# Performance work log

Measured on AMD Instinct MI355X. Metric: run time of the kernel, lower is better.

## Reference

```python
import jax, jax.numpy as jnp
import numpy as np

N_ENT = 50000
N_REL = 500
N_EDGE = 640000
D_IN = 128
D_OUT = 128
NEG_SLOPE = 0.01  # torch nn.LeakyReLU default
BN_EPS = 1e-5


def setup_inputs() -> dict:
    key = jax.random.key(0)
    ks = jax.random.split(key, 16)
    edge_index = jax.random.randint(ks[0], (2, N_EDGE), 0, N_ENT)
    edge_type = jax.random.randint(ks[1], (N_EDGE,), 0, N_REL)
    query_type = jax.random.randint(ks[2], (N_EDGE,), 0, N_REL)
    entity_embed = jax.random.normal(ks[3], (N_ENT, D_IN), jnp.float32)
    rel_embed = jax.random.normal(ks[4], (N_REL, D_IN), jnp.float32)
    s = 0.05
    return {
        "edge_index": edge_index,
        "edge_type": edge_type,
        "query_type": query_type,
        "entity_embed": entity_embed,
        "rel_embed": rel_embed,
        "w_loop": jax.random.normal(ks[5], (D_IN, D_OUT), jnp.float32) * s,
        "w_out": jax.random.normal(ks[6], (D_IN, D_OUT), jnp.float32) * s,
        "w_rel": jax.random.normal(ks[7], (D_IN, D_OUT), jnp.float32) * s,
        "loop_rel": jax.random.normal(ks[8], (1, D_IN), jnp.float32) * s,
        "W_w": jax.random.normal(ks[9], (D_IN, D_IN), jnp.float32) * s,   # W.weight^T layout: x @ W_w
        "W_b": jnp.zeros((D_IN,), jnp.float32),
        "a_w": jax.random.normal(ks[10], (2 * D_IN, 1), jnp.float32) * s,
        "a_b": jnp.zeros((1,), jnp.float32),
        "bias": jnp.zeros((D_OUT,), jnp.float32),
        "bn_gamma": jnp.ones((D_OUT,), jnp.float32),
        "bn_beta": jnp.zeros((D_OUT,), jnp.float32),
    }


def _compgcn_fwd(edge_index, edge_type, query_type, entity_embed, rel_embed,
                 w_loop, w_out, w_rel, loop_rel, W_w, W_b, a_w, a_b,
                 bias, bn_gamma, bn_beta):
    N = entity_embed.shape[0]
    rel_all = jnp.concatenate([rel_embed, loop_rel], axis=0)  # (R+1, D)
    row, col = edge_index[0], edge_index[1]  # values already in [0, N)

    # edge norm: 1/out-degree of source node (deg[row] >= 1 for every edge)
    deg = jax.ops.segment_sum(jnp.ones((row.shape[0],), entity_embed.dtype), row, num_segments=N)
    norm = 1.0 / deg[row]  # (E,)

    # self-loop branch (mode='loop'): rel_transform 'mult' with loop relation, no attention
    loop_res = (entity_embed * rel_all[-1]) @ w_loop  # (N, D_out)

    # out branch (mode='out')
    x_j = entity_embed[col]          # (E, D)
    r_e = rel_all[edge_type]         # (E, D)
    q_e = rel_all[query_type]        # (E, D)
    xj_rel = x_j * r_e               # 'mult' composition

    h = jnp.concatenate([r_e @ W_w + W_b, q_e @ W_w + W_b], axis=-1)  # (E, 2D)
    logits = h @ a_w + a_b                                            # (E, 1)
    alpha = jnp.exp(jax.nn.leaky_relu(logits[:, 0], NEG_SLOPE))       # (E,)
    sum_alpha = jax.ops.segment_sum(alpha, row, num_segments=N)       # (N,)
    alpha = alpha / sum_alpha[row]

    msg = (xj_rel @ w_out) * (alpha * norm)[:, None]                  # (E, D_out)
    out_res = jax.ops.segment_sum(msg, row, num_segments=N)           # (N, D_out)

    out = 0.5 * out_res + 0.5 * loop_res + bias  # dropout = identity (eval)
    # BatchNorm1d, training-mode batch statistics (biased var), over node dim
    mean = jnp.mean(out, axis=0)
    var = jnp.mean((out - mean) ** 2, axis=0)
    out = (out - mean) * jax.lax.rsqrt(var + BN_EPS) * bn_gamma + bn_beta

    ent_out = jax.nn.leaky_relu(out, NEG_SLOPE)
    rel_out = (rel_all @ w_rel)[:-1]
    return ent_out, rel_out


def reference(edge_index, edge_type, query_type, entity_embed, rel_embed,
              w_loop, w_out, w_rel, loop_rel, W_w, W_b, a_w, a_b,
              bias, bn_gamma, bn_beta):
    return _compgcn_fwd(edge_index, edge_type, query_type, entity_embed, rel_embed,
                        w_loop, w_out, w_rel, loop_rel, W_w, W_b, a_w, a_b,
                        bias, bn_gamma, bn_beta)
```

## Files before the change

kernel.cpp:

```cpp
#include <hip/hip_runtime.h>
#include <math.h>

#define E_N 640000
#define N_N 50000
#define R_N 500
#define D   128
#define NEG 0.01f
#define BNEPS 1e-5f
#define CAP 48
#define GROUPS 8
#define RPG 6250

typedef __bf16 bf16x8 __attribute__((ext_vector_type(8)));
typedef float f32x4 __attribute__((ext_vector_type(4)));

#define CNT_OFF    0u
#define STAT_OFF   50000u
#define ZERO_FLOATS 50256u
#define BUCKET_OFF 50256u
#define ENTBF_OFF  4850256u
#define RELBF_OFF  8050256u
#define BT_OFF     8082256u
#define S1_OFF     8098640u
#define S2_OFF     8099152u

__device__ __forceinline__ float lrelu(float x) { return x > 0.f ? x : NEG * x; }

__device__ __forceinline__ void st_bf16x4(__bf16* p, float x, float y, float z, float w) {
    union { __bf16 b[4]; uint2 u; } pk;
    pk.b[0] = (__bf16)x; pk.b[1] = (__bf16)y; pk.b[2] = (__bf16)z; pk.b[3] = (__bf16)w;
    *(uint2*)p = pk.u;
}

__device__ __forceinline__ void st_bf16x8(__bf16* p, const float* v) {
    union { __bf16 b[8]; uint4 u; } pk;
#pragma unroll
    for (int j = 0; j < 8; ++j) pk.b[j] = (__bf16)v[j];
    *(uint4*)p = pk.u;
}

__device__ __forceinline__ void fma8(uint4 ue, uint4 ur, float a, float* acc) {
    const unsigned* we = (const unsigned*)&ue;
    const unsigned* wr = (const unsigned*)&ur;
#pragma unroll
    for (int w = 0; w < 4; ++w) {
        float e_lo = __uint_as_float(we[w] << 16);
        float e_hi = __uint_as_float(we[w] & 0xffff0000u);
        float r_lo = __uint_as_float(wr[w] << 16);
        float r_hi = __uint_as_float(wr[w] & 0xffff0000u);
        acc[2 * w]     = fmaf(a * e_lo, r_lo, acc[2 * w]);
        acc[2 * w + 1] = fmaf(a * e_hi, r_hi, acc[2 * w + 1]);
    }
}

#define P1_S   501
#define P1_WB  256
#define P1_REL 500
#define P1_ENT 1563

__global__ __launch_bounds__(128) void k_pre1(const float* __restrict__ Ww,
                                              const float* __restrict__ Wb,
                                              const float* __restrict__ aw,
                                              const float* __restrict__ rel,
                                              const float* __restrict__ looprel,
                                              const float* __restrict__ wout,
                                              const float* __restrict__ wloop,
                                              const float* __restrict__ wrel,
                                              const float* __restrict__ ent,
                                              float* __restrict__ s1,
                                              float* __restrict__ s2,
                                              __bf16* __restrict__ Bt,
                                              float* __restrict__ out_rel,
                                              __bf16* __restrict__ rel_bf,
                                              __bf16* __restrict__ ent_bf) {
    int b = blockIdx.x, t = threadIdx.x;
    if (b < P1_S) {
        __shared__ float rr[D];
        __shared__ float part[4];
        const float* rp = (b < R_N) ? rel + (size_t)b * D : looprel;
        rr[t] = rp[t];
        if (b < R_N) rel_bf[(size_t)b * D + t] = (__bf16)rp[t];
        __syncthreads();
        float v = 0.f;
        for (int i = 0; i < D; ++i) v = fmaf(rr[i], Ww[i * D + t], v);
        float p1 = aw[t] * v + Wb[t] * aw[t];
        float p2 = aw[D + t] * v + Wb[t] * aw[D + t];
        for (int o = 32; o; o >>= 1) {
            p1 += __shfl_down(p1, o);
            p2 += __shfl_down(p2, o);
        }
        if ((t & 63) == 0) {
            part[(t >> 6) * 2] = p1;
            part[(t >> 6) * 2 + 1] = p2;
        }
        __syncthreads();
        if (t == 0) {
            s1[b] = part[0] + part[2];
            s2[b] = part[1] + part[3];
        }
    } else if (b < P1_S + P1_WB) {
        int idx = (b - P1_S) * 128 + t;
        int n = idx & 127, k = idx >> 7;
        float v = (k < D) ? wout[(size_t)k * D + n] : wloop[(size_t)(k - D) * D + n];
        Bt[(size_t)n * 256 + k] = (__bf16)v;
    } else if (b < P1_S + P1_WB + P1_REL) {
        int r = b - (P1_S + P1_WB);
        __shared__ float rr2[D];
        rr2[t] = rel[(size_t)r * D + t];
        __syncthreads();
        float a = 0.f;
        for (int k = 0; k < D; ++k) a = fmaf(rr2[k], wrel[(size_t)k * D + t], a);
        out_rel[(size_t)r * D + t] = a;
    } else {
        int blk = b - (P1_S + P1_WB + P1_REL);
        const float4* e4 = (const float4*)ent;
#pragma unroll
        for (int j = 0; j < 8; ++j) {
            int idx = blk * 1024 + j * 128 + t;
            if (idx < N_N * D / 4) {
                float4 v = e4[idx];
                st_bf16x4(ent_bf + (size_t)idx * 4, v.x, v.y, v.z, v.w);
            }
        }
    }
}

#define BIN_BLOCKS (625 * GROUPS)

__global__ __launch_bounds__(256) void k_bin(const int* __restrict__ row,
                                             const int* __restrict__ col,
                                             const int* __restrict__ et,
                                             const int* __restrict__ qt,
                                             const float* __restrict__ s1,
                                             const float* __restrict__ s2,
                                             const float* __restrict__ ab,
                                             int* __restrict__ cnt,
                                             int2* __restrict__ bucket) {
    int b = blockIdx.x, t = threadIdx.x;
    int g = b & 7;
    int chunk = b >> 3;
    int rlo = g * RPG;
    int e0 = chunk * 1024 + t;
    int r[4];
#pragma unroll
    for (int j = 0; j < 4; ++j) r[j] = row[e0 + j * 256];
#pragma unroll
    for (int j = 0; j < 4; ++j) {
        unsigned rr = (unsigned)(r[j] - rlo);
        if (rr < RPG) {
            int e = e0 + j * 256;
            int c = col[e], te = et[e], q = qt[e];
            float a = __expf(lrelu(s1[te] + s2[q] + ab[0]));
            int pos = atomicAdd(&cnt[r[j]], 1);
            if (pos < CAP) {
                bucket[(size_t)r[j] * CAP + pos] =
                    make_int2(c | (te << 16), __float_as_int(a));
            }
        }
    }
}

__global__ __launch_bounds__(128) void k_gather(const int* __restrict__ cnt,
                                                const int2* __restrict__ bucket,
                                                const __bf16* __restrict__ ent_bf,
                                                const __bf16* __restrict__ rel_bf,
                                                const float* __restrict__ looprel,
                                                __bf16* __restrict__ stage) {
    int n = (blockIdx.x & 7) * RPG + (blockIdx.x >> 3);
    int t = threadIdx.x;
    int deg = cnt[n];
    int m = deg < CAP ? deg : CAP;
    __shared__ int eoff[CAP];
    __shared__ int roff[CAP];
    __shared__ float sa[CAP];
    __shared__ float xred[16][8];
    if (t < CAP) {
        if (t < m) {
            int2 be = bucket[(size_t)n * CAP + t];
            eoff[t] = (be.x & 0xffff) << 8;
            roff[t] = (be.x >> 16) << 8;
            sa[t] = __int_as_float(be.y);
        } else {
            eoff[t] = 0; roff[t] = 0; sa[t] = 0.f;
        }
    }
    __syncthreads();
    float suma = 0.f;
    for (int i = 0; i < m; ++i) suma += sa[i];
    int s = t & 15, g = t >> 4;
    const char* eb = (const char*)ent_bf;
    const char* rb = (const char*)rel_bf;
    int co = s * 16;
    float acc[8] = {0, 0, 0, 0, 0, 0, 0, 0};
#define EDGE(e_) { \
        uint4 ue = *(const uint4*)(eb + (eoff[e_] + co)); \
        uint4 ur = *(const uint4*)(rb + (roff[e_] + co)); \
        fma8(ue, ur, sa[e_], acc); }
    EDGE(g) EDGE(g + 8)
    if (m > 16) { EDGE(g + 16) EDGE(g + 24) }
    if (m > 32) { EDGE(g + 32) EDGE(g + 40) }
#undef EDGE
#pragma unroll
    for (int k = 0; k < 8; ++k) {
        acc[k] += __shfl_xor(acc[k], 16);
        acc[k] += __shfl_xor(acc[k], 32);
    }
    if (t >= 64 && t < 80) {
#pragma unroll
        for (int k = 0; k < 8; ++k) xred[s][k] = acc[k];
    }
    if (t >= 96 && t < 112) {
        int si = t - 96;
        uint4 ue = *(const uint4*)(eb + ((size_t)n << 8) + si * 16);
        const unsigned* we = (const unsigned*)&ue;
        float v[8];
#pragma unroll
        for (int w = 0; w < 4; ++w) {
            v[2 * w]     = __uint_as_float(we[w] << 16) * looprel[si * 8 + 2 * w];
            v[2 * w + 1] = __uint_as_float(we[w] & 0xffff0000u) * looprel[si * 8 + 2 * w + 1];
        }
        st_bf16x8(stage + (size_t)n * 256 + 128 + si * 8, v);
    }
    __syncthreads();
    if (t < 16) {
        float inv = (deg > 0) ? 1.0f / (suma * (float)deg) : 0.f;
        float v[8];
#pragma unroll
        for (int k = 0; k < 8; ++k) v[k] = (acc[k] + xred[s][k]) * inv;
        st_bf16x8(stage + (size_t)n * 256 + s * 8, v);
    }
}

__global__ __launch_bounds__(256) void k_gemm(const __bf16* stage,
                                              const __bf16* __restrict__ Bt,
                                              const float* __restrict__ bias,
                                              float* out,
                                              float* __restrict__ stat) {
    int t = threadIdx.x;
    int wave = t >> 6, l = t & 63;
    int lm = l & 15, lg = l >> 4;
    size_t mbase = (size_t)blockIdx.x * 128 + wave * 32;
    const bf16x8* A = (const bf16x8*)stage;
    const bf16x8* B = (const bf16x8*)Bt;
    f32x4 acc[2][8];
#pragma unroll
    for (int mt = 0; mt < 2; ++mt)
#pragma unroll
        for (int nt = 0; nt < 8; ++nt) acc[mt][nt] = (f32x4)(0.f);
#pragma unroll
    for (int ks = 0; ks < 8; ++ks) {
        bf16x8 a0 = A[(mbase + lm) * 32 + ks * 4 + lg];
        bf16x8 a1 = A[(mbase + 16 + lm) * 32 + ks * 4 + lg];
#pragma unroll
        for (int nt = 0; nt < 8; ++nt) {
            bf16x8 b = B[(size_t)(nt * 16 + lm) * 32 + ks * 4 + lg];
            acc[0][nt] = __builtin_amdgcn_mfma_f32_16x16x32_bf16(a0, b, acc[0][nt], 0, 0, 0);
            acc[1][nt] = __builtin_amdgcn_mfma_f32_16x16x32_bf16(a1, b, acc[1][nt], 0, 0, 0);
        }
    }
    float psum[8], psq[8];
#pragma unroll
    for (int nt = 0; nt < 8; ++nt) { psum[nt] = 0.f; psq[nt] = 0.f; }
#pragma unroll
    for (int mt = 0; mt < 2; ++mt) {
#pragma unroll
        for (int nt = 0; nt < 8; ++nt) {
            int c = nt * 16 + lm;
            float bv = bias[c];
#pragma unroll
            for (int r = 0; r < 4; ++r) {
                size_t rowi = mbase + mt * 16 + lg * 4 + r;
                if (rowi < N_N) {
                    float v = 0.5f * acc[mt][nt][r] + bv;
                    out[rowi * D + c] = v;
                    psum[nt] += v;
                    psq[nt] += v * v;
                }
            }
        }
    }
    __shared__ float2 red[8][16][16];
    int slot = wave * 4 + lg;
#pragma unroll
    for (int nt = 0; nt < 8; ++nt) red[nt][lm][slot] = make_float2(psum[nt], psq[nt]);
    __syncthreads();
    if (t < 128) {
        int nt = t >> 4, lmm = t & 15;
        float ss = 0.f, qq = 0.f;
#pragma unroll
        for (int k = 0; k < 16; ++k) {
            float2 v = red[nt][lmm][k];
            ss += v.x;
            qq += v.y;
        }
        atomicAdd(&stat[t], ss);
        atomicAdd(&stat[D + t], qq);
    }
}

__global__ __launch_bounds__(256) void k_bnapply(float* __restrict__ out,
                                                 const float* __restrict__ stat,
                                                 const float* __restrict__ gamma,
                                                 const float* __restrict__ beta) {
    __shared__ float ssc[D], ssh[D];
    int t = threadIdx.x;
    if (t < D) {
        float mean = stat[t] * (1.0f / N_N);
        float var = stat[D + t] * (1.0f / N_N) - mean * mean;
        float sc = gamma[t] * rsqrtf(var + BNEPS);
        ssc[t] = sc;
        ssh[t] = beta[t] - mean * sc;
    }
    __syncthreads();
    const float4* sc4 = (const float4*)ssc;
    const float4* sh4 = (const float4*)ssh;
    float4* o4 = (float4*)out;
    const int total = N_N * D / 4;
    for (int i = blockIdx.x * blockDim.x + t; i < total; i += gridDim.x * blockDim.x) {
        int d4 = i & 31;
        float4 v = o4[i];
        float4 s = sc4[d4];
        float4 h = sh4[d4];
        v.x = lrelu(v.x * s.x + h.x);
        v.y = lrelu(v.y * s.y + h.y);
        v.z = lrelu(v.z * s.z + h.z);
        v.w = lrelu(v.w * s.w + h.w);
        o4[i] = v;
    }
}

extern "C" void kernel_launch(void* const* d_in, const int* in_sizes, int n_in,
                              void* d_out, int out_size, void* d_ws, size_t ws_size,
                              hipStream_t stream) {
    const int* edge_index = (const int*)d_in[0];
    const int* row = edge_index;
    const int* col = edge_index + E_N;
    const int* etype = (const int*)d_in[1];
    const int* qtype = (const int*)d_in[2];
    const float* ent = (const float*)d_in[3];
    const float* rel = (const float*)d_in[4];
    const float* w_loop = (const float*)d_in[5];
    const float* w_out = (const float*)d_in[6];
    const float* w_rel = (const float*)d_in[7];
    const float* loop_rel = (const float*)d_in[8];
    const float* W_w = (const float*)d_in[9];
    const float* W_b = (const float*)d_in[10];
    const float* a_w = (const float*)d_in[11];
    const float* a_b = (const float*)d_in[12];
    const float* bias = (const float*)d_in[13];
    const float* bn_gamma = (const float*)d_in[14];
    const float* bn_beta = (const float*)d_in[15];

    float* ws = (float*)d_ws;
    int* cnt = (int*)(ws + CNT_OFF);
    float* stat = ws + STAT_OFF;
    int2* bucket = (int2*)(ws + BUCKET_OFF);
    __bf16* ent_bf = (__bf16*)(ws + ENTBF_OFF);
    __bf16* rel_bf = (__bf16*)(ws + RELBF_OFF);
    __bf16* Bt = (__bf16*)(ws + BT_OFF);
    float* s1 = ws + S1_OFF;
    float* s2 = ws + S2_OFF;

    float* out_ent = (float*)d_out;
    float* out_rel = out_ent + (size_t)N_N * D;
    __bf16* stage = (__bf16*)d_out;

    hipMemsetAsync(d_ws, 0, (size_t)ZERO_FLOATS * sizeof(float), stream);

    k_pre1<<<P1_S + P1_WB + P1_REL + P1_ENT, 128, 0, stream>>>(
        W_w, W_b, a_w, rel, loop_rel, w_out, w_loop, w_rel, ent,
        s1, s2, Bt, out_rel, rel_bf, ent_bf);
    k_bin<<<BIN_BLOCKS, 256, 0, stream>>>(
        row, col, etype, qtype, s1, s2, a_b, cnt, bucket);
    k_gather<<<N_N, 128, 0, stream>>>(cnt, bucket, ent_bf, rel_bf, loop_rel, stage);
    k_gemm<<<(N_N + 127) / 128, 256, 0, stream>>>(stage, Bt, bias, out_ent, stat);
    k_bnapply<<<2048, 256, 0, stream>>>(out_ent, stat, bn_gamma, bn_beta);
}
```

Measured before the change: 136.5 us.

## Widen gather lanes to 32B and store pre-BN activations as bf16 intermediate

The gather kernel now has each lane handle 16 features as two 16-byte loads, with 16 edge groups per block instead of 8 and an extra shuffle-reduction step. The GEMM epilogue writes pre-BatchNorm values into a bf16 workspace buffer instead of fp32 in the output. BN-apply then reads bf16 and writes fp32, which cuts the intermediate round-trip traffic. In exchange, the pre-BN activations are rounded to bf16 before normalization, adding some precision loss. Because of aliasing, the stage buffer still lives in d_out.

```diff
diff --git a/kernel.cpp b/kernel.cpp
--- a/kernel.cpp
+++ b/kernel.cpp
@@ -23,6 +23,7 @@
 #define BT_OFF     8082256u
 #define S1_OFF     8098640u
 #define S2_OFF     8099152u
+#define MID_OFF    8099664u
 
 __device__ __forceinline__ float lrelu(float x) { return x > 0.f ? x : NEG * x; }
 
@@ -173,7 +174,7 @@
     __shared__ int eoff[CAP];
     __shared__ int roff[CAP];
     __shared__ float sa[CAP];
-    __shared__ float xred[16][8];
+    __shared__ float xred[8][16];
     if (t < CAP) {
         if (t < m) {
             int2 be = bucket[(size_t)n * CAP + t];
@@ -187,54 +188,65 @@
     __syncthreads();
     float suma = 0.f;
     for (int i = 0; i < m; ++i) suma += sa[i];
-    int s = t & 15, g = t >> 4;
+    int s = t & 7, g = t >> 3;
     const char* eb = (const char*)ent_bf;
     const char* rb = (const char*)rel_bf;
-    int co = s * 16;
-    float acc[8] = {0, 0, 0, 0, 0, 0, 0, 0};
+    int co = s * 32;
+    float acc[16];
+#pragma unroll
+    for (int k = 0; k < 16; ++k) acc[k] = 0.f;
 #define EDGE(e_) { \
-        uint4 ue = *(const uint4*)(eb + (eoff[e_] + co)); \
-        uint4 ur = *(const uint4*)(rb + (roff[e_] + co)); \
-        fma8(ue, ur, sa[e_], acc); }
-    EDGE(g) EDGE(g + 8)
-    if (m > 16) { EDGE(g + 16) EDGE(g + 24) }
-    if (m > 32) { EDGE(g + 32) EDGE(g + 40) }
+        uint4 ue0 = *(const uint4*)(eb + (eoff[e_] + co)); \
+        uint4 ue1 = *(const uint4*)(eb + (eoff[e_] + co + 16)); \
+        uint4 ur0 = *(const uint4*)(rb + (roff[e_] + co)); \
+        uint4 ur1 = *(const uint4*)(rb + (roff[e_] + co + 16)); \
+        fma8(ue0, ur0, sa[e_], acc); \
+        fma8(ue1, ur1, sa[e_], acc + 8); }
+    EDGE(g) EDGE(g + 16)
+    if (m > 32) EDGE(g + 32)
 #undef EDGE
 #pragma unroll
-    for (int k = 0; k < 8; ++k) {
+    for (int k = 0; k < 16; ++k) {
+        acc[k] += __shfl_xor(acc[k], 8);
         acc[k] += __shfl_xor(acc[k], 16);
         acc[k] += __shfl_xor(acc[k], 32);
     }
-    if (t >= 64 && t < 80) {
-#pragma unroll
-        for (int k = 0; k < 8; ++k) xred[s][k] = acc[k];
-    }
-    if (t >= 96 && t < 112) {
-        int si = t - 96;
-        uint4 ue = *(const uint4*)(eb + ((size_t)n << 8) + si * 16);
-        const unsigned* we = (const unsigned*)&ue;
-        float v[8];
+    if (t >= 64 && t < 72) {
+#pragma unroll
+        for (int k = 0; k < 16; ++k) xred[s][k] = acc[k];
+    }
+    if (t >= 72 && t < 80) {
+        int si = t - 72;
+        uint4 u0 = *(const uint4*)(eb + ((size_t)n << 8) + si * 32);
+        uint4 u1 = *(const uint4*)(eb + ((size_t)n << 8) + si * 32 + 16);
+        const unsigned* w0 = (const unsigned*)&u0;
+        const unsigned* w1 = (const unsigned*)&u1;
+        float v[16];
 #pragma unroll
         for (int w = 0; w < 4; ++w) {
-            v[2 * w]     = __uint_as_float(we[w] << 16) * looprel[si * 8 + 2 * w];
-            v[2 * w + 1] = __uint_as_float(we[w] & 0xffff0000u) * looprel[si * 8 + 2 * w + 1];
-        }
-        st_bf16x8(stage + (size_t)n * 256 + 128 + si * 8, v);
+            v[2 * w]     = __uint_as_float(w0[w] << 16) * looprel[si * 16 + 2 * w];
+            v[2 * w + 1] = __uint_as_float(w0[w] & 0xffff0000u) * looprel[si * 16 + 2 * w + 1];
+            v[8 + 2 * w]     = __uint_as_float(w1[w] << 16) * looprel[si * 16 + 8 + 2 * w];
+            v[8 + 2 * w + 1] = __uint_as_float(w1[w] & 0xffff0000u) * looprel[si * 16 + 8 + 2 * w + 1];
+        }
+        st_bf16x8(stage + (size_t)n * 256 + 128 + si * 16, v);
+        st_bf16x8(stage + (size_t)n * 256 + 128 + si * 16 + 8, v + 8);
     }
     __syncthreads();
-    if (t < 16) {
+    if (t < 8) {
         float inv = (deg > 0) ? 1.0f / (suma * (float)deg) : 0.f;
-        float v[8];
-#pragma unroll
-        for (int k = 0; k < 8; ++k) v[k] = (acc[k] + xred[s][k]) * inv;
-        st_bf16x8(stage + (size_t)n * 256 + s * 8, v);
-    }
-}
-
-__global__ __launch_bounds__(256) void k_gemm(const __bf16* stage,
+        float v[16];
+#pragma unroll
+        for (int k = 0; k < 16; ++k) v[k] = (acc[k] + xred[t][k]) * inv;
+        st_bf16x8(stage + (size_t)n * 256 + t * 16, v);
+        st_bf16x8(stage + (size_t)n * 256 + t * 16 + 8, v + 8);
+    }
+}
+
+__global__ __launch_bounds__(256) void k_gemm(const __bf16* __restrict__ stage,
                                               const __bf16* __restrict__ Bt,
                                               const float* __restrict__ bias,
-                                              float* out,
+                                              __bf16* __restrict__ mid,
                                               float* __restrict__ stat) {
     int t = threadIdx.x;
     int wave = t >> 6, l = t & 63;
@@ -272,7 +284,7 @@
                 size_t rowi = mbase + mt * 16 + lg * 4 + r;
                 if (rowi < N_N) {
                     float v = 0.5f * acc[mt][nt][r] + bv;
-                    out[rowi * D + c] = v;
+                    mid[rowi * D + c] = (__bf16)v;
                     psum[nt] += v;
                     psq[nt] += v * v;
                 }
@@ -298,7 +310,8 @@
     }
 }
 
-__global__ __launch_bounds__(256) void k_bnapply(float* __restrict__ out,
+__global__ __launch_bounds__(256) void k_bnapply(const __bf16* __restrict__ mid,
+                                                 float* __restrict__ out,
                                                  const float* __restrict__ stat,
                                                  const float* __restrict__ gamma,
                                                  const float* __restrict__ beta) {
@@ -312,20 +325,26 @@
         ssh[t] = beta[t] - mean * sc;
     }
     __syncthreads();
-    const float4* sc4 = (const float4*)ssc;
-    const float4* sh4 = (const float4*)ssh;
+    const uint4* m4 = (const uint4*)mid;
     float4* o4 = (float4*)out;
-    const int total = N_N * D / 4;
-    for (int i = blockIdx.x * blockDim.x + t; i < total; i += gridDim.x * blockDim.x) {
-        int d4 = i & 31;
-        float4 v = o4[i];
-        float4 s = sc4[d4];
-        float4 h = sh4[d4];
-        v.x = lrelu(v.x * s.x + h.x);
-        v.y = lrelu(v.y * s.y + h.y);
-        v.z = lrelu(v.z * s.z + h.z);
-        v.w = lrelu(v.w * s.w + h.w);
-        o4[i] = v;
+    const int total8 = N_N * D / 8;
+    for (int i = blockIdx.x * blockDim.x + t; i < total8; i += gridDim.x * blockDim.x) {
+        int c0 = (i & 15) * 8;
+        uint4 u = m4[i];
+        const unsigned* w = (const unsigned*)&u;
+        float4 r0, r1;
+        float vv[8];
+#pragma unroll
+        for (int j = 0; j < 4; ++j) {
+            vv[2 * j]     = __uint_as_float(w[j] << 16);
+            vv[2 * j + 1] = __uint_as_float(w[j] & 0xffff0000u);
+        }
+#pragma unroll
+        for (int j = 0; j < 8; ++j) vv[j] = lrelu(vv[j] * ssc[c0 + j] + ssh[c0 + j]);
+        r0 = make_float4(vv[0], vv[1], vv[2], vv[3]);
+        r1 = make_float4(vv[4], vv[5], vv[6], vv[7]);
+        o4[2 * i] = r0;
+        o4[2 * i + 1] = r1;
     }
 }
 
@@ -360,6 +379,7 @@
     __bf16* Bt = (__bf16*)(ws + BT_OFF);
     float* s1 = ws + S1_OFF;
     float* s2 = ws + S2_OFF;
+    __bf16* mid = (__bf16*)(ws + MID_OFF);
 
     float* out_ent = (float*)d_out;
     float* out_rel = out_ent + (size_t)N_N * D;
@@ -373,6 +393,6 @@
     k_bin<<<BIN_BLOCKS, 256, 0, stream>>>(
         row, col, etype, qtype, s1, s2, a_b, cnt, bucket);
     k_gather<<<N_N, 128, 0, stream>>>(cnt, bucket, ent_bf, rel_bf, loop_rel, stage);
-    k_gemm<<<(N_N + 127) / 128, 256, 0, stream>>>(stage, Bt, bias, out_ent, stat);
-    k_bnapply<<<2048, 256, 0, stream>>>(out_ent, stat, bn_gamma, bn_beta);
-}
+    k_gemm<<<(N_N + 127) / 128, 256, 0, stream>>>(stage, Bt, bias, mid, stat);
+    k_bnapply<<<2048, 256, 0, stream>>>(mid, out_ent, stat, bn_gamma, bn_beta);
+}
```

New measurement: 171.1 us. 1.25x slower.
